# Performance work log

Measured on AMD Instinct MI355X. Metric: run time of the kernel, lower is better.

## Reference

```python
import jax, jax.numpy as jnp
import numpy as np
from jax import lax

MAX_SCALE = 4
SCALES = [2 ** i for i in range(1, MAX_SCALE + 1)]  # [2, 4, 8, 16]
EPS = 1e-6
BN_EPS = 1e-3  # keras BatchNormalization default epsilon


def _box_sum(x, r):
    # DepthwiseConv2D with ones kernel, SAME zero padding == box sum window
    return lax.reduce_window(x, 0.0, lax.add, (1, r, r, 1), (1, 1, 1, 1), 'SAME')


def setup_inputs() -> dict:
    key = jax.random.key(0)
    k1, k2 = jax.random.split(key)
    B, H, W, C, K = 4, 224, 224, 64, 8
    return {
        'x': jax.random.normal(k1, (B, H, W, C), dtype=jnp.float32),
        'ols_weights': jnp.ones((MAX_SCALE,), jnp.float32),
        'anchors': jax.random.normal(k2, (C, K), dtype=jnp.float32),
        'hist_widths': jnp.ones((C, K), jnp.float32),
        'bn_gamma': jnp.ones((C,), jnp.float32),
        'bn_beta': jnp.zeros((C,), jnp.float32),
        'bn_mean': jnp.zeros((C,), jnp.float32),
        'bn_var': jnp.ones((C,), jnp.float32),
    }


def reference(x, ols_weights, anchors, hist_widths, bn_gamma, bn_beta, bn_mean, bn_var):
    # --- sample min-max scaling to [0, 1] per sample ---
    xmin = jnp.min(x, axis=(1, 2, 3), keepdims=True)
    xmax = jnp.max(x, axis=(1, 2, 3), keepdims=True)
    xs = (x - xmin) / (xmax - xmin + EPS)

    # --- multi-scale box measures: [B,H,W,C,S] ---
    measures = jnp.stack([_box_sum(xs, r) for r in SCALES], axis=-1)

    # --- weighted OLS slope of log(measure) vs log(scale) -> local alpha ---
    ly = jnp.log(measures + EPS)                         # [B,H,W,C,S]
    lr = jnp.log(jnp.asarray(SCALES, jnp.float32))       # [S]
    w = ols_weights                                       # [S]
    wsum = jnp.sum(w)
    lr_bar = jnp.sum(w * lr) / wsum
    ly_bar = jnp.sum(w * ly, axis=-1, keepdims=True) / wsum
    dx = lr - lr_bar                                      # [S]
    num = jnp.sum(w * dx * (ly - ly_bar), axis=-1)        # [B,H,W,C]
    den = jnp.sum(w * dx * dx)
    alphas = num / den

    # --- batch norm (inference mode, training=False) ---
    a = bn_gamma * (alphas - bn_mean) * lax.rsqrt(bn_var + BN_EPS) + bn_beta

    # --- triangular soft histogram over k anchors, relu'd and summed ---
    hist = 1.0 - hist_widths * jnp.abs(a[..., None] - anchors)  # [B,H,W,C,K]
    soft_counts = jnp.sum(jax.nn.relu(hist), axis=-1)           # [B,H,W,C]

    return x + jax.nn.sigmoid(soft_counts)
```

## Files before the change

kernel.cpp:

```cpp
#include <hip/hip_runtime.h>
#include <math.h>

#define B 4
#define H 224
#define W 224
#define C 64
#define K 8
#define WC (W*C)
#define HWC (H*W*C)

__device__ inline float wave_reduce_min(float v) {
  #pragma unroll
  for (int off = 32; off > 0; off >>= 1)
    v = fminf(v, __shfl_down(v, off, 64));
  return v;
}
__device__ inline float wave_reduce_max(float v) {
  #pragma unroll
  for (int off = 32; off > 0; off >>= 1)
    v = fmaxf(v, __shfl_down(v, off, 64));
  return v;
}

__global__ __launch_bounds__(256) void k_minmax_part(const float* __restrict__ x,
                                                     float* __restrict__ scratch) {
  int s   = blockIdx.x >> 7;
  int blk = blockIdx.x & 127;
  const float4* xs = (const float4*)(x + (size_t)s * HWC);
  const int n4 = HWC / 4;
  float vmin = INFINITY, vmax = -INFINITY;
  for (int i = blk*256 + threadIdx.x; i < n4; i += 128*256) {
    float4 v = xs[i];
    vmin = fminf(vmin, fminf(fminf(v.x, v.y), fminf(v.z, v.w)));
    vmax = fmaxf(vmax, fmaxf(fmaxf(v.x, v.y), fmaxf(v.z, v.w)));
  }
  __shared__ float smin[4], smax[4];
  float wmin = wave_reduce_min(vmin), wmax = wave_reduce_max(vmax);
  int wave = threadIdx.x >> 6, lane = threadIdx.x & 63;
  if (lane == 0) { smin[wave] = wmin; smax[wave] = wmax; }
  __syncthreads();
  if (threadIdx.x == 0) {
    float m = fminf(fminf(smin[0], smin[1]), fminf(smin[2], smin[3]));
    float M = fmaxf(fmaxf(smax[0], smax[1]), fmaxf(smax[2], smax[3]));
    scratch[blockIdx.x]       = m;
    scratch[512 + blockIdx.x] = M;
  }
}

__global__ __launch_bounds__(128) void k_minmax_final(float* __restrict__ scratch) {
  int s = blockIdx.x;
  float vmin = scratch[s*128 + threadIdx.x];
  float vmax = scratch[512 + s*128 + threadIdx.x];
  __shared__ float smin[2], smax[2];
  float wmin = wave_reduce_min(vmin), wmax = wave_reduce_max(vmax);
  int wave = threadIdx.x >> 6, lane = threadIdx.x & 63;
  if (lane == 0) { smin[wave] = wmin; smax[wave] = wmax; }
  __syncthreads();
  if (threadIdx.x == 0) {
    float m = fminf(smin[0], smin[1]);
    float M = fmaxf(smax[0], smax[1]);
    scratch[1024 + s] = m;
    scratch[1028 + s] = 1.0f / (M - m + 1e-6f);
  }
}

__global__ __launch_bounds__(512) void k_prefix(const float* __restrict__ x,
                                                const float* __restrict__ scratch,
                                                float* __restrict__ P) {
  int bid = blockIdx.x;
  int b = bid / W, w = bid % W;
  int q = threadIdx.x >> 6, c = threadIdx.x & 63;
  float xmin = scratch[1024 + b];
  float inv  = scratch[1028 + b];
  size_t colbase = (size_t)b*HWC + (size_t)w*C + c;
  const int hq = q * 28;
  const float* xp = x + colbase + (size_t)hq * WC;

  float v[28];
  #pragma unroll
  for (int j = 0; j < 28; ++j) v[j] = xp[(size_t)j * WC];
  float sum = 0.f;
  #pragma unroll
  for (int j = 0; j < 28; ++j) sum += v[j];

  __shared__ float lds[512];
  lds[threadIdx.x] = sum;
  __syncthreads();

  float acc = 0.f;
  for (int qq = 0; qq < q; ++qq) acc += lds[qq*64 + c];

  float* Pp = P + colbase + (size_t)hq * WC;
  #pragma unroll
  for (int j = 0; j < 28; ++j) {
    acc += v[j];
    Pp[(size_t)j * WC] = (acc - (float)(hq + j + 1) * xmin) * inv;
  }
}

__global__ __launch_bounds__(128) void k_main(
    const float* __restrict__ P, const float* __restrict__ x,
    const float* __restrict__ ols, const float* __restrict__ anchors,
    const float* __restrict__ hwidths, const float* __restrict__ bn_gamma,
    const float* __restrict__ bn_beta, const float* __restrict__ bn_mean,
    const float* __restrict__ bn_var, float* __restrict__ out) {
  int xcd  = blockIdx.x & 7;
  int i    = blockIdx.x >> 3;
  int rg   = xcd * 112 + (i >> 2);
  int wave = threadIdx.x >> 6, c = threadIdx.x & 63;
  int chunk = (i & 3) * 2 + wave;
  int b = rg / H, h = rg % H;
  int w0 = chunk * 28;

  const float LN2 = 0.69314718055994530942f;
  float wg0 = ols[0], wg1 = ols[1], wg2 = ols[2], wg3 = ols[3];
  float l0 = LN2, l1 = 2.f*LN2, l2 = 3.f*LN2, l3 = 4.f*LN2;
  float wsum = wg0 + wg1 + wg2 + wg3;
  float lrbar = (wg0*l0 + wg1*l1 + wg2*l2 + wg3*l3) / wsum;
  float d0 = l0-lrbar, d1 = l1-lrbar, d2 = l2-lrbar, d3 = l3-lrbar;
  float den = wg0*d0*d0 + wg1*d1*d1 + wg2*d2*d2 + wg3*d3*d3;
  float c0 = wg0*d0/den, c1 = wg1*d1/den, c2 = wg2*d2/den, c3 = wg3*d3/den;

  float scl  = bn_gamma[c] * rsqrtf(bn_var[c] + 1e-3f);
  float bofs = bn_beta[c] - bn_mean[c] * scl;
  float anc[K], wd[K];
  #pragma unroll
  for (int k = 0; k < K; ++k) { anc[k] = anchors[c*K + k]; wd[k] = hwidths[c*K + k]; }

  const int hiA[4] = {1, 2, 4, 8};
  const int loA[4] = {0, 1, 3, 7};
  const float* pt[4]; const float* pb[4]; float fb[4];
  #pragma unroll
  for (int s = 0; s < 4; ++s) {
    int ht = h + hiA[s]; if (ht > H-1) ht = H-1;
    int hb = h - loA[s] - 1;
    int hbc = hb < 0 ? 0 : hb;
    pt[s] = P + (size_t)b*HWC + (size_t)ht*WC + c;
    pb[s] = P + (size_t)b*HWC + (size_t)hbc*WC + c;
    fb[s] = hb < 0 ? 0.f : 1.f;
  }

  const float* xrow = x   + (size_t)b*HWC + (size_t)h*WC + c;
  float*       orow = out + (size_t)b*HWC + (size_t)h*WC + c;

  float ring2[2]   = {0,0};
  float ring4[4]   = {0,0,0,0};
  float ring8[8]   = {0,0,0,0,0,0,0,0};
  float ring16[16] = {0,0,0,0,0,0,0,0,0,0,0,0,0,0,0,0};
  float T0 = 0.f, T1 = 0.f, T2 = 0.f, T3 = 0.f;
  float abuf[8] = {0,0,0,0,0,0,0,0};

  for (int t0 = 0; t0 < 48; t0 += 16) {
    #pragma unroll
    for (int u = 0; u < 16; ++u) {
      int t  = t0 + u;
      int wr = w0 - 7 + t;
      float m0 = 0.f, m1 = 0.f, m2 = 0.f, m3 = 0.f;
      if (wr >= 0 && wr < W) {
        int off = wr * C;
        m0 = pt[0][off] - fb[0]*pb[0][off];
        m1 = pt[1][off] - fb[1]*pb[1][off];
        m2 = pt[2][off] - fb[2]*pb[2][off];
        m3 = pt[3][off] - fb[3]*pb[3][off];
      }
      T0 += m0 - ring2[u&1];  ring2[u&1]  = m0;
      T1 += m1 - ring4[u&3];  ring4[u&3]  = m1;
      T2 += m2 - ring8[u&7];  ring8[u&7]  = m2;
      T3 += m3 - ring16[u];   ring16[u]   = m3;
      abuf[(u+7)&7] += c0 * __logf(fmaxf(T0, 0.f) + 1e-6f);
      abuf[(u+6)&7] += c1 * __logf(fmaxf(T1, 0.f) + 1e-6f);
      abuf[(u+4)&7] += c2 * __logf(fmaxf(T2, 0.f) + 1e-6f);
      abuf[u&7]     += c3 * __logf(fmaxf(T3, 0.f) + 1e-6f);
      int ig = w0 - 15 + t;
      if (t >= 15 && ig <= w0 + 27) {
        float alpha = abuf[u&7];
        float a = alpha * scl + bofs;
        float sc = 0.f;
        #pragma unroll
        for (int k = 0; k < K; ++k)
          sc += fmaxf(0.f, 1.f - wd[k]*fabsf(a - anc[k]));
        float sig = 1.f / (1.f + __expf(-sc));
        float xv = __builtin_nontemporal_load(&xrow[ig*C]);
        __builtin_nontemporal_store(xv + sig, &orow[ig*C]);
      }
      abuf[u&7] = 0.f;
    }
  }
}

extern "C" void kernel_launch(void* const* d_in, const int* in_sizes, int n_in,
                              void* d_out, int out_size, void* d_ws, size_t ws_size,
                              hipStream_t stream) {
  const float* x        = (const float*)d_in[0];
  const float* ols      = (const float*)d_in[1];
  const float* anchors  = (const float*)d_in[2];
  const float* hwidths  = (const float*)d_in[3];
  const float* bn_gamma = (const float*)d_in[4];
  const float* bn_beta  = (const float*)d_in[5];
  const float* bn_mean  = (const float*)d_in[6];
  const float* bn_var   = (const float*)d_in[7];
  float* out = (float*)d_out;
  float* P   = (float*)d_ws;
  float* scratch = out;

  hipLaunchKernelGGL(k_minmax_part,  dim3(512),     dim3(256), 0, stream, x, scratch);
  hipLaunchKernelGGL(k_minmax_final, dim3(4),       dim3(128), 0, stream, scratch);
  hipLaunchKernelGGL(k_prefix,       dim3(B*W),     dim3(512), 0, stream, x, scratch, P);
  hipLaunchKernelGGL(k_main,         dim3(B*H*4),   dim3(128), 0, stream,
                     P, x, ols, anchors, hwidths, bn_gamma, bn_beta, bn_mean, bn_var, out);
}
```

Measured before the change: 220.8 us.

## Batch main-loop loads ahead of compute and simplify column prefix kernel

The main kernel now issues the top, bottom and x loads for a group of four columns before doing their compute, with edge indices clamped and masked by a multiplier instead of branched. This is meant to raise memory-level parallelism and hide load latency. Base pointers become wave-uniform through readfirstlane, and launch bounds request higher occupancy. The prefix kernel becomes one sequential scan per column over all 224 rows in 448 small blocks, removing the LDS cross-quarter combine but leaving far fewer waves in flight to cover latency.

```diff
diff --git a/kernel.cpp b/kernel.cpp
--- a/kernel.cpp
+++ b/kernel.cpp
@@ -64,41 +64,32 @@
   }
 }
 
-__global__ __launch_bounds__(512) void k_prefix(const float* __restrict__ x,
-                                                const float* __restrict__ scratch,
-                                                float* __restrict__ P) {
+__global__ __launch_bounds__(128) void k_vpfx(const float* __restrict__ x,
+                                              const float* __restrict__ scratch,
+                                              float* __restrict__ P) {
   int bid = blockIdx.x;
-  int b = bid / W, w = bid % W;
-  int q = threadIdx.x >> 6, c = threadIdx.x & 63;
+  int b = bid / 112, wt = bid % 112;
+  int w = wt * 2 + (threadIdx.x >> 6);
+  int c = threadIdx.x & 63;
   float xmin = scratch[1024 + b];
   float inv  = scratch[1028 + b];
-  size_t colbase = (size_t)b*HWC + (size_t)w*C + c;
-  const int hq = q * 28;
-  const float* xp = x + colbase + (size_t)hq * WC;
-
-  float v[28];
-  #pragma unroll
-  for (int j = 0; j < 28; ++j) v[j] = xp[(size_t)j * WC];
-  float sum = 0.f;
-  #pragma unroll
-  for (int j = 0; j < 28; ++j) sum += v[j];
-
-  __shared__ float lds[512];
-  lds[threadIdx.x] = sum;
-  __syncthreads();
-
+  const float* xb = x + __builtin_amdgcn_readfirstlane(b * HWC);
+  float*       Pb = P + __builtin_amdgcn_readfirstlane(b * HWC);
+  int lbase = w * C + c;
   float acc = 0.f;
-  for (int qq = 0; qq < q; ++qq) acc += lds[qq*64 + c];
-
-  float* Pp = P + colbase + (size_t)hq * WC;
-  #pragma unroll
-  for (int j = 0; j < 28; ++j) {
-    acc += v[j];
-    Pp[(size_t)j * WC] = (acc - (float)(hq + j + 1) * xmin) * inv;
-  }
-}
-
-__global__ __launch_bounds__(128) void k_main(
+  for (int j0 = 0; j0 < H; j0 += 16) {
+    float v[16];
+    #pragma unroll
+    for (int u = 0; u < 16; ++u) v[u] = xb[lbase + (j0 + u) * WC];
+    #pragma unroll
+    for (int u = 0; u < 16; ++u) {
+      acc = fmaf(v[u] - xmin, inv, acc);
+      Pb[lbase + (j0 + u) * WC] = acc;
+    }
+  }
+}
+
+__global__ __launch_bounds__(128, 4) void k_main(
     const float* __restrict__ P, const float* __restrict__ x,
     const float* __restrict__ ols, const float* __restrict__ anchors,
     const float* __restrict__ hwidths, const float* __restrict__ bn_gamma,
@@ -130,18 +121,18 @@
   const int hiA[4] = {1, 2, 4, 8};
   const int loA[4] = {0, 1, 3, 7};
   const float* pt[4]; const float* pb[4]; float fb[4];
+  int base_b = b * HWC;
   #pragma unroll
   for (int s = 0; s < 4; ++s) {
     int ht = h + hiA[s]; if (ht > H-1) ht = H-1;
     int hb = h - loA[s] - 1;
     int hbc = hb < 0 ? 0 : hb;
-    pt[s] = P + (size_t)b*HWC + (size_t)ht*WC + c;
-    pb[s] = P + (size_t)b*HWC + (size_t)hbc*WC + c;
+    pt[s] = P + __builtin_amdgcn_readfirstlane(base_b + ht * WC);
+    pb[s] = P + __builtin_amdgcn_readfirstlane(base_b + hbc * WC);
     fb[s] = hb < 0 ? 0.f : 1.f;
   }
-
-  const float* xrow = x   + (size_t)b*HWC + (size_t)h*WC + c;
-  float*       orow = out + (size_t)b*HWC + (size_t)h*WC + c;
+  const float* xrow = x   + __builtin_amdgcn_readfirstlane(base_b + h * WC);
+  float*       orow = out + __builtin_amdgcn_readfirstlane(base_b + h * WC);
 
   float ring2[2]   = {0,0};
   float ring4[4]   = {0,0,0,0};
@@ -152,38 +143,51 @@
 
   for (int t0 = 0; t0 < 48; t0 += 16) {
     #pragma unroll
-    for (int u = 0; u < 16; ++u) {
-      int t  = t0 + u;
-      int wr = w0 - 7 + t;
-      float m0 = 0.f, m1 = 0.f, m2 = 0.f, m3 = 0.f;
-      if (wr >= 0 && wr < W) {
-        int off = wr * C;
-        m0 = pt[0][off] - fb[0]*pb[0][off];
-        m1 = pt[1][off] - fb[1]*pb[1][off];
-        m2 = pt[2][off] - fb[2]*pb[2][off];
-        m3 = pt[3][off] - fb[3]*pb[3][off];
+    for (int g = 0; g < 4; ++g) {
+      float lt[4][4], lb[4][4], lx[4];
+      #pragma unroll
+      for (int j = 0; j < 4; ++j) {
+        int t  = t0 + g*4 + j;
+        int wr = w0 - 7 + t;
+        int wrc = wr < 0 ? 0 : (wr > W-1 ? W-1 : wr);
+        int off = wrc * C + c;
+        #pragma unroll
+        for (int s = 0; s < 4; ++s) { lt[j][s] = pt[s][off]; lb[j][s] = pb[s][off]; }
+        int ig  = w0 - 15 + t;
+        int igc = ig < 0 ? 0 : (ig > W-1 ? W-1 : ig);
+        lx[j] = __builtin_nontemporal_load(&xrow[igc * C + c]);
       }
-      T0 += m0 - ring2[u&1];  ring2[u&1]  = m0;
-      T1 += m1 - ring4[u&3];  ring4[u&3]  = m1;
-      T2 += m2 - ring8[u&7];  ring8[u&7]  = m2;
-      T3 += m3 - ring16[u];   ring16[u]   = m3;
-      abuf[(u+7)&7] += c0 * __logf(fmaxf(T0, 0.f) + 1e-6f);
-      abuf[(u+6)&7] += c1 * __logf(fmaxf(T1, 0.f) + 1e-6f);
-      abuf[(u+4)&7] += c2 * __logf(fmaxf(T2, 0.f) + 1e-6f);
-      abuf[u&7]     += c3 * __logf(fmaxf(T3, 0.f) + 1e-6f);
-      int ig = w0 - 15 + t;
-      if (t >= 15 && ig <= w0 + 27) {
-        float alpha = abuf[u&7];
-        float a = alpha * scl + bofs;
-        float sc = 0.f;
-        #pragma unroll
-        for (int k = 0; k < K; ++k)
-          sc += fmaxf(0.f, 1.f - wd[k]*fabsf(a - anc[k]));
-        float sig = 1.f / (1.f + __expf(-sc));
-        float xv = __builtin_nontemporal_load(&xrow[ig*C]);
-        __builtin_nontemporal_store(xv + sig, &orow[ig*C]);
+      #pragma unroll
+      for (int j = 0; j < 4; ++j) {
+        int u = g*4 + j;
+        int t = t0 + u;
+        int wr = w0 - 7 + t;
+        float fw = (wr >= 0 && wr < W) ? 1.f : 0.f;
+        float m0 = fw * fmaf(-fb[0], lb[j][0], lt[j][0]);
+        float m1 = fw * fmaf(-fb[1], lb[j][1], lt[j][1]);
+        float m2 = fw * fmaf(-fb[2], lb[j][2], lt[j][2]);
+        float m3 = fw * fmaf(-fb[3], lb[j][3], lt[j][3]);
+        T0 += m0 - ring2[u&1];  ring2[u&1]  = m0;
+        T1 += m1 - ring4[u&3];  ring4[u&3]  = m1;
+        T2 += m2 - ring8[u&7];  ring8[u&7]  = m2;
+        T3 += m3 - ring16[u];   ring16[u]   = m3;
+        abuf[(u+7)&7] += c0 * __logf(fmaxf(T0, 0.f) + 1e-6f);
+        abuf[(u+6)&7] += c1 * __logf(fmaxf(T1, 0.f) + 1e-6f);
+        abuf[(u+4)&7] += c2 * __logf(fmaxf(T2, 0.f) + 1e-6f);
+        abuf[u&7]     += c3 * __logf(fmaxf(T3, 0.f) + 1e-6f);
+        if (t >= 15 && t <= 42) {
+          int ig = w0 - 15 + t;
+          float alpha = abuf[u&7];
+          float a = alpha * scl + bofs;
+          float sc = 0.f;
+          #pragma unroll
+          for (int k = 0; k < K; ++k)
+            sc += fmaxf(0.f, 1.f - wd[k]*fabsf(a - anc[k]));
+          float sig = 1.f / (1.f + __expf(-sc));
+          __builtin_nontemporal_store(lx[j] + sig, &orow[ig*C + c]);
+        }
+        abuf[u&7] = 0.f;
       }
-      abuf[u&7] = 0.f;
     }
   }
 }
@@ -203,9 +207,9 @@
   float* P   = (float*)d_ws;
   float* scratch = out;
 
-  hipLaunchKernelGGL(k_minmax_part,  dim3(512),     dim3(256), 0, stream, x, scratch);
-  hipLaunchKernelGGL(k_minmax_final, dim3(4),       dim3(128), 0, stream, scratch);
-  hipLaunchKernelGGL(k_prefix,       dim3(B*W),     dim3(512), 0, stream, x, scratch, P);
-  hipLaunchKernelGGL(k_main,         dim3(B*H*4),   dim3(128), 0, stream,
+  hipLaunchKernelGGL(k_minmax_part,  dim3(512),   dim3(256), 0, stream, x, scratch);
+  hipLaunchKernelGGL(k_minmax_final, dim3(4),     dim3(128), 0, stream, scratch);
+  hipLaunchKernelGGL(k_vpfx,         dim3(448),   dim3(128), 0, stream, x, scratch, P);
+  hipLaunchKernelGGL(k_main,         dim3(B*H*4), dim3(128), 0, stream,
                      P, x, ols, anchors, hwidths, bn_gamma, bn_beta, bn_mean, bn_var, out);
 }
```

Result: slower. 226.1 us (+2.4%).
